# Performance work log

Hardware: AMD Instinct MI355X
Metric: run time of the kernel (lower is better)

The kernel has to match this reference:

```python
import jax, jax.numpy as jnp
import numpy as np

A = 20.0  # sigmoid sharpness used by the module

def norm_sigmoid(x):
    # module's sigmoid: min/max normalize over the whole tensor, then steep sigmoid
    xn = (x - jnp.min(x)) / (jnp.max(x) - jnp.min(x))
    return jax.nn.sigmoid(A * xn)

def setup_inputs() -> dict:
    key = jax.random.key(0)
    ks = jax.random.split(key, 10)
    B, T = 2048, 512
    input_dim, nh1, nh2, nh3, output_dim = 1, 256, 256, 128, 1
    def lin(k, fan_in, fan_out):
        bound = 1.0 / np.sqrt(fan_in)
        kw, kb = jax.random.split(k)
        W = jax.random.uniform(kw, (fan_out, fan_in), jnp.float32, -bound, bound)
        b = jax.random.uniform(kb, (fan_out,), jnp.float32, -bound, bound)
        return W, b
    W1, b1 = lin(ks[0], input_dim, nh1)
    W2, b2 = lin(ks[1], nh1, nh2)
    W4, b4 = lin(ks[2], nh3, output_dim)
    j_w = jax.random.normal(ks[3], (nh3,), jnp.float32)
    k_w = jax.random.normal(ks[4], (nh3,), jnp.float32)
    X = jax.random.normal(ks[5], (B, T), jnp.float32)
    return {"X": X, "W1": W1, "b1": b1, "W2": W2, "b2": b2,
            "W4": W4, "b4": b4, "j_w": j_w, "k_w": k_w}

def reference(X, W1, b1, W2, b2, W4, b4, j_w, k_w):
    B, T = X.shape
    nh3 = j_w.shape[0]
    xs = jnp.swapaxes(X, 0, 1)[:, :, None]  # [T, B, 1] scalar input per step

    def step(state, x_t):
        out1 = norm_sigmoid(x_t @ W1.T + b1)          # [B, nh1]
        out2 = norm_sigmoid(out1 @ W2.T + b2)         # [B, nh2]
        j, k = out2[:, :nh3], out2[:, nh3:]
        inp_j = norm_sigmoid(j * j_w)
        inp_k = norm_sigmoid(k * k_w)
        new_state = (1.0 - state) * inp_j + (1.0 - inp_k) * state  # flip-flop update
        out4 = norm_sigmoid(new_state @ W4.T + b4)    # [B, 1]
        return new_state, out4

    state0 = jnp.zeros((B, nh3), X.dtype)
    _, ys = jax.lax.scan(step, state0, xs)            # ys: [T, B, 1]
    return jnp.squeeze(jnp.swapaxes(ys, 0, 1), axis=2)  # [B, T]
```

## Files before the change

### kernel.cpp

```cpp
#include <hip/hip_runtime.h>

#define TT 512
#define BB 2048
#define HH 256

typedef _Float16 f16x8 __attribute__((ext_vector_type(8)));
typedef _Float16 f16x4 __attribute__((ext_vector_type(4)));
typedef float f32x4 __attribute__((ext_vector_type(4)));

__device__ __forceinline__ float sigf(float z) {
    return __builtin_amdgcn_rcpf(1.0f + __expf(-z));
}
__device__ __forceinline__ unsigned f2o(float f) {
    unsigned u = __float_as_uint(f);
    return (u & 0x80000000u) ? ~u : (u | 0x80000000u);
}
__device__ __forceinline__ float o2f(unsigned o) {
    unsigned u = (o & 0x80000000u) ? (o & 0x7fffffffu) : ~o;
    return __uint_as_float(u);
}

__global__ __launch_bounds__(256) void k0_stats(const float* __restrict__ X,
                                                const float* __restrict__ W1,
                                                const float* __restrict__ b1,
                                                float* __restrict__ mn1f, float* __restrict__ s1f,
                                                unsigned* __restrict__ colGmn,
                                                unsigned* __restrict__ colGmx,
                                                float2* __restrict__ statep) {
    int t = blockIdx.x, tid = threadIdx.x;
    statep[blockIdx.x * 256 + tid] = make_float2(0.f, 0.f);
    colGmn[(size_t)t * 256 + tid] = 0xFFFFFFFFu;
    colGmx[(size_t)t * 256 + tid] = 0u;
    __shared__ float rmn[256], rmx[256];
    float mn = 3.4e38f, mx = -3.4e38f;
    for (int b = tid; b < BB; b += 256) {
        float v = X[(size_t)b * TT + t];
        mn = fminf(mn, v); mx = fmaxf(mx, v);
    }
    rmn[tid] = mn; rmx[tid] = mx; __syncthreads();
    for (int s = 128; s > 0; s >>= 1) {
        if (tid < s) { rmn[tid] = fminf(rmn[tid], rmn[tid + s]); rmx[tid] = fmaxf(rmx[tid], rmx[tid + s]); }
        __syncthreads();
    }
    float xmn = rmn[0], xmx = rmx[0];
    __syncthreads();
    float w = W1[tid], bb = b1[tid];
    float v0 = w * xmn + bb, v1 = w * xmx + bb;
    rmn[tid] = fminf(v0, v1); rmx[tid] = fmaxf(v0, v1); __syncthreads();
    for (int s = 128; s > 0; s >>= 1) {
        if (tid < s) { rmn[tid] = fminf(rmn[tid], rmn[tid + s]); rmx[tid] = fmaxf(rmx[tid], rmx[tid + s]); }
        __syncthreads();
    }
    if (tid == 0) {
        mn1f[t] = rmn[0];
        s1f[t] = 20.0f / (rmx[0] - rmn[0]);
    }
}

__global__ __launch_bounds__(256) void k0b_cvt(const float* __restrict__ W2,
                                               _Float16* __restrict__ W2hi) {
    int i4 = (blockIdx.x * 256 + threadIdx.x) * 4;
    float4 v = *(const float4*)&W2[i4];
    f16x4 h;
    h[0] = (_Float16)v.x; h[1] = (_Float16)v.y; h[2] = (_Float16)v.z; h[3] = (_Float16)v.w;
    *(f16x4*)&W2hi[i4] = h;
}

__global__ __launch_bounds__(256) void k1_gemm(const float* __restrict__ X,
                                               const float* __restrict__ W1,
                                               const float* __restrict__ b1,
                                               const _Float16* __restrict__ W2h,
                                               const float* __restrict__ b2,
                                               const float* __restrict__ mn1f,
                                               const float* __restrict__ s1f,
                                               float* __restrict__ buf,
                                               unsigned* __restrict__ colGmn,
                                               unsigned* __restrict__ colGmx,
                                               int tbase) {
    int tl = blockIdx.z, t = tbase + tl;
    int bBase = blockIdx.x * 64;
    int tid = threadIdx.x;
    __shared__ __align__(16) _Float16 A[2][64 * 256];
    float* C_lds = (float*)A;
    int lane = tid & 63, w = tid >> 6;
    int l15 = lane & 15, hi2 = lane >> 4;

    {
        int sr = tid >> 2, ks0 = (tid & 3) * 64;
        float xr = X[(size_t)(bBase + sr) * TT + t];
        float mn1 = mn1f[t], s1 = s1f[t];
#pragma unroll
        for (int g = 0; g < 8; ++g) {
            int k = ks0 + g * 8;
            float4 wa = *(const float4*)&W1[k];
            float4 wb = *(const float4*)&W1[k + 4];
            float4 ba = *(const float4*)&b1[k];
            float4 bb = *(const float4*)&b1[k + 4];
            float av[8];
            av[0] = sigf((xr * wa.x + ba.x - mn1) * s1);
            av[1] = sigf((xr * wa.y + ba.y - mn1) * s1);
            av[2] = sigf((xr * wa.z + ba.z - mn1) * s1);
            av[3] = sigf((xr * wa.w + ba.w - mn1) * s1);
            av[4] = sigf((xr * wb.x + bb.x - mn1) * s1);
            av[5] = sigf((xr * wb.y + bb.y - mn1) * s1);
            av[6] = sigf((xr * wb.z + bb.z - mn1) * s1);
            av[7] = sigf((xr * wb.w + bb.w - mn1) * s1);
            f16x8 hv, lv;
#pragma unroll
            for (int u = 0; u < 8; ++u) {
                _Float16 ah = (_Float16)av[u];
                hv[u] = ah;
                lv[u] = (_Float16)(av[u] - (float)ah);
            }
            int kgs = (k >> 3) ^ (sr & 7);
            *(f16x8*)&A[0][sr * 256 + kgs * 8] = hv;
            *(f16x8*)&A[1][sr * 256 + kgs * 8] = lv;
        }
    }
    __syncthreads();

    f32x4 acc[4][4];
#pragma unroll
    for (int i = 0; i < 4; ++i)
#pragma unroll
        for (int j = 0; j < 4; ++j) acc[i][j] = (f32x4)0.0f;

    const _Float16* bp[4];
#pragma unroll
    for (int j = 0; j < 4; ++j)
        bp[j] = W2h + (size_t)(w * 64 + j * 16 + l15) * HH + hi2 * 8;

#pragma unroll
    for (int s = 0; s < 8; ++s) {
        f16x8 bh[4];
#pragma unroll
        for (int j = 0; j < 4; ++j) bh[j] = *(const f16x8*)(bp[j] + s * 32);
#pragma unroll
        for (int i = 0; i < 4; ++i) {
            int row = i * 16 + l15;
            int kgs = (s * 4 + hi2) ^ (row & 7);
            f16x8 ah = *(const f16x8*)&A[0][row * 256 + kgs * 8];
            f16x8 al = *(const f16x8*)&A[1][row * 256 + kgs * 8];
#pragma unroll
            for (int j = 0; j < 4; ++j) {
                acc[i][j] = __builtin_amdgcn_mfma_f32_16x16x32_f16(al, bh[j], acc[i][j], 0, 0, 0);
                acc[i][j] = __builtin_amdgcn_mfma_f32_16x16x32_f16(ah, bh[j], acc[i][j], 0, 0, 0);
            }
        }
    }

    float b2r[4];
#pragma unroll
    for (int j = 0; j < 4; ++j) b2r[j] = b2[w * 64 + j * 16 + l15];
#pragma unroll
    for (int j = 0; j < 4; ++j) {
        float vmn = 3.4e38f, vmx = -3.4e38f;
#pragma unroll
        for (int i = 0; i < 4; ++i)
#pragma unroll
            for (int q = 0; q < 4; ++q) {
                float v = acc[i][j][q] + b2r[j];
                acc[i][j][q] = v;
                vmn = fminf(vmn, v); vmx = fmaxf(vmx, v);
            }
        vmn = fminf(vmn, __shfl_xor(vmn, 16)); vmn = fminf(vmn, __shfl_xor(vmn, 32));
        vmx = fmaxf(vmx, __shfl_xor(vmx, 16)); vmx = fmaxf(vmx, __shfl_xor(vmx, 32));
        if (hi2 == 0) {
            int c = w * 64 + j * 16 + l15;
            atomicMin(&colGmn[(size_t)t * 256 + c], f2o(vmn));
            atomicMax(&colGmx[(size_t)t * 256 + c], f2o(vmx));
        }
    }
    __syncthreads();
#pragma unroll
    for (int i = 0; i < 4; ++i)
#pragma unroll
        for (int j = 0; j < 4; ++j)
#pragma unroll
            for (int q = 0; q < 4; ++q)
                C_lds[(i * 16 + hi2 * 4 + q) * 256 + w * 64 + j * 16 + l15] = acc[i][j][q];
    __syncthreads();
#pragma unroll
    for (int it = 0; it < 16; ++it) {
        int idx = it * 256 + tid;
        int row = idx >> 6, g = idx & 63;
        float4 v = *(const float4*)&C_lds[row * 256 + g * 4];
        *(float4*)&buf[((size_t)tl * BB + bBase + row) * HH + g * 4] = v;
    }
}

__global__ __launch_bounds__(256) void k1b(const unsigned* __restrict__ colGmn,
                                           const unsigned* __restrict__ colGmx,
                                           const float* __restrict__ j_w,
                                           const float* __restrict__ k_w,
                                           float* __restrict__ mn2f, float* __restrict__ s2f,
                                           float* __restrict__ mjf, float* __restrict__ sjf,
                                           float* __restrict__ mkf, float* __restrict__ skf,
                                           int tbase) {
    int t = tbase + blockIdx.x, tid = threadIdx.x;
    __shared__ float ra[256], rb[256];
    float cmn = o2f(colGmn[(size_t)t * 256 + tid]);
    float cmx = o2f(colGmx[(size_t)t * 256 + tid]);
    ra[tid] = cmn; rb[tid] = cmx; __syncthreads();
    for (int s = 128; s > 0; s >>= 1) {
        if (tid < s) { ra[tid] = fminf(ra[tid], ra[tid + s]); rb[tid] = fmaxf(rb[tid], rb[tid + s]); }
        __syncthreads();
    }
    float mn2 = ra[0], mx2 = rb[0];
    float s2 = 20.0f / (mx2 - mn2);
    __syncthreads();
    float wv = (tid < 128) ? j_w[tid] : k_w[tid - 128];
    float ea = sigf((cmn - mn2) * s2) * wv;
    float eb = sigf((cmx - mn2) * s2) * wv;
    ra[tid] = fminf(ea, eb); rb[tid] = fmaxf(ea, eb); __syncthreads();
    for (int s = 64; s > 0; s >>= 1) {
        if ((tid & 127) < s) { ra[tid] = fminf(ra[tid], ra[tid + s]); rb[tid] = fmaxf(rb[tid], rb[tid + s]); }
        __syncthreads();
    }
    if (tid == 0) {
        mn2f[t] = mn2; s2f[t] = s2;
        mjf[t] = ra[0]; sjf[t] = 20.0f / (rb[0] - ra[0]);
    }
    if (tid == 128) {
        mkf[t] = ra[128]; skf[t] = 20.0f / (rb[128] - ra[128]);
    }
}

__global__ __launch_bounds__(256) void k3_scan(const float* __restrict__ buf,
                                               const float* __restrict__ W4,
                                               const float* __restrict__ b4,
                                               const float* __restrict__ mn2f, const float* __restrict__ s2f,
                                               const float* __restrict__ mjf, const float* __restrict__ sjf,
                                               const float* __restrict__ mkf, const float* __restrict__ skf,
                                               const float* __restrict__ j_w, const float* __restrict__ k_w,
                                               float2* __restrict__ statep,
                                               float* __restrict__ out4p,
                                               int tbase, int TC) {
    __shared__ float n2L[512], c2L[512], mjL[512], sjL[512], mkL[512], skL[512];
    int tid = threadIdx.x;
    for (int tl = tid; tl < TC; tl += 256) {
        int t = tbase + tl;
        n2L[tl] = mn2f[t]; c2L[tl] = s2f[t];
        mjL[tl] = mjf[t]; sjL[tl] = sjf[t];
        mkL[tl] = mkf[t]; skL[tl] = skf[t];
    }
    __syncthreads();
    int wave = tid >> 6, lane = tid & 63;
    int b = blockIdx.x * 4 + wave;
    float w40 = W4[2 * lane], w41 = W4[2 * lane + 1];
    float jw0 = j_w[2 * lane], jw1 = j_w[2 * lane + 1];
    float kw0 = k_w[2 * lane], kw1 = k_w[2 * lane + 1];
    float bb4 = b4[0];
    float2 stv = statep[b * 64 + lane];
    float s0 = stv.x, s1v = stv.y;
    const float2* basep = (const float2*)buf;
    const int rowstride = BB * 128;
    int off0 = b * 128 + lane;
    float rsave = 0.f;
    float2 jq[8], kq[8];
#pragma unroll
    for (int u = 0; u < 8; ++u) {
        jq[u] = basep[(size_t)u * rowstride + off0];
        kq[u] = basep[(size_t)u * rowstride + off0 + 64];
    }
    for (int t0 = 0; t0 < TC; t0 += 8) {
#pragma unroll
        for (int u = 0; u < 8; ++u) {
            int tl = t0 + u;
            float2 jp = jq[u], kp = kq[u];
            int tn = tl + 8;
            if (tn < TC) {
                jq[u] = basep[(size_t)tn * rowstride + off0];
                kq[u] = basep[(size_t)tn * rowstride + off0 + 64];
            }
            float n2 = n2L[tl], c2 = c2L[tl];
            float pj0 = sigf((jp.x - n2) * c2) * jw0;
            float pj1 = sigf((jp.y - n2) * c2) * jw1;
            float pk0 = sigf((kp.x - n2) * c2) * kw0;
            float pk1 = sigf((kp.y - n2) * c2) * kw1;
            float ij0 = sigf((pj0 - mjL[tl]) * sjL[tl]);
            float ij1 = sigf((pj1 - mjL[tl]) * sjL[tl]);
            float ik0 = sigf((pk0 - mkL[tl]) * skL[tl]);
            float ik1 = sigf((pk1 - mkL[tl]) * skL[tl]);
            s0 = ij0 + s0 * (1.0f - ij0 - ik0);
            s1v = ij1 + s1v * (1.0f - ij1 - ik1);
            float r = s0 * w40 + s1v * w41;
#pragma unroll
            for (int m = 1; m < 64; m <<= 1) r += __shfl_xor(r, m);
            if (lane == (tl & 63)) rsave = r + bb4;
        }
        if (((t0 + 8) & 63) == 0) {
            int base = t0 + 8 - 64;
            out4p[(size_t)b * TT + tbase + base + lane] = rsave;
        }
    }
    if (TC < 64 && lane < TC) out4p[(size_t)b * TT + tbase + lane] = rsave;
    statep[b * 64 + lane] = make_float2(s0, s1v);
}

__global__ __launch_bounds__(256) void k3b(const float* __restrict__ out4p,
                                           float* __restrict__ mn4f, float* __restrict__ s4f) {
    int t = blockIdx.x, tid = threadIdx.x;
    __shared__ float rmn[256], rmx[256];
    float mn = 3.4e38f, mx = -3.4e38f;
    for (int b = tid; b < BB; b += 256) {
        float v = out4p[(size_t)b * TT + t];
        mn = fminf(mn, v); mx = fmaxf(mx, v);
    }
    rmn[tid] = mn; rmx[tid] = mx; __syncthreads();
    for (int s = 128; s > 0; s >>= 1) {
        if (tid < s) { rmn[tid] = fminf(rmn[tid], rmn[tid + s]); rmx[tid] = fmaxf(rmx[tid], rmx[tid + s]); }
        __syncthreads();
    }
    if (tid == 0) { mn4f[t] = rmn[0]; s4f[t] = 20.0f / (rmx[0] - rmn[0]); }
}

__global__ __launch_bounds__(256) void k4_final(float* __restrict__ out,
                                                const float* __restrict__ mn4f,
                                                const float* __restrict__ s4f) {
    int i = blockIdx.x * 256 + threadIdx.x;
    float4 v = ((const float4*)out)[i];
    int t0 = (i * 4) & (TT - 1);
    float4 mn = *(const float4*)&mn4f[t0];
    float4 sc = *(const float4*)&s4f[t0];
    float4 r;
    r.x = sigf((v.x - mn.x) * sc.x);
    r.y = sigf((v.y - mn.y) * sc.y);
    r.z = sigf((v.z - mn.z) * sc.z);
    r.w = sigf((v.w - mn.w) * sc.w);
    ((float4*)out)[i] = r;
}

extern "C" void kernel_launch(void* const* d_in, const int* in_sizes, int n_in,
                              void* d_out, int out_size, void* d_ws, size_t ws_size,
                              hipStream_t stream) {
    const float* X  = (const float*)d_in[0];
    const float* W1 = (const float*)d_in[1];
    const float* b1 = (const float*)d_in[2];
    const float* W2 = (const float*)d_in[3];
    const float* b2 = (const float*)d_in[4];
    const float* W4 = (const float*)d_in[5];
    const float* b4 = (const float*)d_in[6];
    const float* j_w = (const float*)d_in[7];
    const float* k_w = (const float*)d_in[8];
    float* out = (float*)d_out;

    const size_t stateB = (size_t)BB * 64 * sizeof(float2);
    const size_t colGB  = (size_t)TT * 256 * 2 * 4;
    const size_t w2hB   = (size_t)HH * HH * 2;
    const size_t statsB = 65536;
    int TC = 512;
    while (TC > 8 && ((size_t)TC * BB * HH * 4 + stateB + colGB + w2hB + statsB) > ws_size) TC >>= 1;
    int NC = TT / TC;

    char* w = (char*)d_ws;
    float* buf = (float*)w;
    size_t off = (size_t)TC * BB * HH * 4;
    float2* statep = (float2*)(w + off); off += stateB;
    unsigned* colGmn = (unsigned*)(w + off); off += colGB / 2;
    unsigned* colGmx = (unsigned*)(w + off); off += colGB / 2;
    _Float16* W2hi = (_Float16*)(w + off); off += w2hB;
    float* fst = (float*)(w + off);
    float* mn1f = fst;        float* s1f = fst + 512;
    float* mn2f = fst + 1024; float* s2f = fst + 1536;
    float* mjf  = fst + 2048; float* sjf = fst + 2560;
    float* mkf  = fst + 3072; float* skf = fst + 3584;
    float* mn4f = fst + 4096; float* s4f = fst + 4608;
    float* out4p = out;

    k0_stats<<<512, 256, 0, stream>>>(X, W1, b1, mn1f, s1f, colGmn, colGmx, statep);
    k0b_cvt<<<64, 256, 0, stream>>>(W2, W2hi);
    for (int c = 0; c < NC; ++c) {
        int tbase = c * TC;
        k1_gemm<<<dim3(BB / 64, 1, TC), 256, 0, stream>>>(X, W1, b1, W2hi, b2, mn1f, s1f,
                                                          buf, colGmn, colGmx, tbase);
        k1b<<<TC, 256, 0, stream>>>(colGmn, colGmx, j_w, k_w, mn2f, s2f, mjf, sjf, mkf, skf, tbase);
        k3_scan<<<512, 256, 0, stream>>>(buf, W4, b4, mn2f, s2f, mjf, sjf, mkf, skf,
                                         j_w, k_w, statep, out4p, tbase, TC);
    }
    k3b<<<512, 256, 0, stream>>>(out4p, mn4f, s4f);
    k4_final<<<1024, 256, 0, stream>>>(out, mn4f, s4f);
}
```

Measured before the change: 973.9 us.

## Split GEMM K-loop into halves to shrink LDS footprint in k1_gemm

The hi/lo fp16 A staging in k1_gemm is cut from 64KB to half size by processing K in two 128-wide halves, each with its own fill, barrier and MFMA pass. The C write-back now goes through LDS in two 128-column rounds with a padded stride of 132 floats. The aim is to fit within about 33KB of LDS so more blocks can be resident per CU, and the padding should also reduce bank conflicts on the C staging. In exchange the kernel gains extra __syncthreads barriers, and only half the waves do the LDS stores in each epilogue round.

Result: no change. 984.0 us (+1.0%).

```diff
diff --git a/kernel.cpp b/kernel.cpp
--- a/kernel.cpp
+++ b/kernel.cpp
@@ -80,18 +80,35 @@
     int tl = blockIdx.z, t = tbase + tl;
     int bBase = blockIdx.x * 64;
     int tid = threadIdx.x;
-    __shared__ __align__(16) _Float16 A[2][64 * 256];
-    float* C_lds = (float*)A;
+    __shared__ __align__(16) char smem[33792];
+    _Float16* A0 = (_Float16*)smem;
+    _Float16* A1 = A0 + 8192;
+    float* C_lds = (float*)smem;
     int lane = tid & 63, w = tid >> 6;
     int l15 = lane & 15, hi2 = lane >> 4;
 
-    {
-        int sr = tid >> 2, ks0 = (tid & 3) * 64;
-        float xr = X[(size_t)(bBase + sr) * TT + t];
-        float mn1 = mn1f[t], s1 = s1f[t];
-#pragma unroll
-        for (int g = 0; g < 8; ++g) {
-            int k = ks0 + g * 8;
+    int sr = tid >> 2, ks0 = (tid & 3) * 32;
+    float xr = X[(size_t)(bBase + sr) * TT + t];
+    float mn1 = mn1f[t], s1 = s1f[t];
+
+    const _Float16* bp[4];
+#pragma unroll
+    for (int j = 0; j < 4; ++j)
+        bp[j] = W2h + (size_t)(w * 64 + j * 16 + l15) * HH + hi2 * 8;
+
+    f32x4 acc[4][4];
+#pragma unroll
+    for (int i = 0; i < 4; ++i)
+#pragma unroll
+        for (int j = 0; j < 4; ++j) acc[i][j] = (f32x4)0.0f;
+
+#pragma unroll
+    for (int kh = 0; kh < 2; ++kh) {
+        if (kh) __syncthreads();
+#pragma unroll
+        for (int g = 0; g < 4; ++g) {
+            int klocal = ks0 + g * 8;
+            int k = kh * 128 + klocal;
             float4 wa = *(const float4*)&W1[k];
             float4 wb = *(const float4*)&W1[k + 4];
             float4 ba = *(const float4*)&b1[k];
@@ -112,39 +129,27 @@
                 hv[u] = ah;
                 lv[u] = (_Float16)(av[u] - (float)ah);
             }
-            int kgs = (k >> 3) ^ (sr & 7);
-            *(f16x8*)&A[0][sr * 256 + kgs * 8] = hv;
-            *(f16x8*)&A[1][sr * 256 + kgs * 8] = lv;
-        }
-    }
-    __syncthreads();
-
-    f32x4 acc[4][4];
-#pragma unroll
-    for (int i = 0; i < 4; ++i)
-#pragma unroll
-        for (int j = 0; j < 4; ++j) acc[i][j] = (f32x4)0.0f;
-
-    const _Float16* bp[4];
-#pragma unroll
-    for (int j = 0; j < 4; ++j)
-        bp[j] = W2h + (size_t)(w * 64 + j * 16 + l15) * HH + hi2 * 8;
-
-#pragma unroll
-    for (int s = 0; s < 8; ++s) {
-        f16x8 bh[4];
-#pragma unroll
-        for (int j = 0; j < 4; ++j) bh[j] = *(const f16x8*)(bp[j] + s * 32);
-#pragma unroll
-        for (int i = 0; i < 4; ++i) {
-            int row = i * 16 + l15;
-            int kgs = (s * 4 + hi2) ^ (row & 7);
-            f16x8 ah = *(const f16x8*)&A[0][row * 256 + kgs * 8];
-            f16x8 al = *(const f16x8*)&A[1][row * 256 + kgs * 8];
-#pragma unroll
-            for (int j = 0; j < 4; ++j) {
-                acc[i][j] = __builtin_amdgcn_mfma_f32_16x16x32_f16(al, bh[j], acc[i][j], 0, 0, 0);
-                acc[i][j] = __builtin_amdgcn_mfma_f32_16x16x32_f16(ah, bh[j], acc[i][j], 0, 0, 0);
+            int kgs = (klocal >> 3) ^ (sr & 7);
+            *(f16x8*)&A0[sr * 128 + kgs * 8] = hv;
+            *(f16x8*)&A1[sr * 128 + kgs * 8] = lv;
+        }
+        __syncthreads();
+#pragma unroll
+        for (int s = 0; s < 4; ++s) {
+            f16x8 bh[4];
+#pragma unroll
+            for (int j = 0; j < 4; ++j) bh[j] = *(const f16x8*)(bp[j] + kh * 128 + s * 32);
+#pragma unroll
+            for (int i = 0; i < 4; ++i) {
+                int row = i * 16 + l15;
+                int kgs = (s * 4 + hi2) ^ (row & 7);
+                f16x8 ah = *(const f16x8*)&A0[row * 128 + kgs * 8];
+                f16x8 al = *(const f16x8*)&A1[row * 128 + kgs * 8];
+#pragma unroll
+                for (int j = 0; j < 4; ++j) {
+                    acc[i][j] = __builtin_amdgcn_mfma_f32_16x16x32_f16(al, bh[j], acc[i][j], 0, 0, 0);
+                    acc[i][j] = __builtin_amdgcn_mfma_f32_16x16x32_f16(ah, bh[j], acc[i][j], 0, 0, 0);
+                }
             }
         }
     }
@@ -171,21 +176,28 @@
             atomicMax(&colGmx[(size_t)t * 256 + c], f2o(vmx));
         }
     }
-    __syncthreads();
-#pragma unroll
-    for (int i = 0; i < 4; ++i)
-#pragma unroll
-        for (int j = 0; j < 4; ++j)
-#pragma unroll
-            for (int q = 0; q < 4; ++q)
-                C_lds[(i * 16 + hi2 * 4 + q) * 256 + w * 64 + j * 16 + l15] = acc[i][j][q];
-    __syncthreads();
-#pragma unroll
-    for (int it = 0; it < 16; ++it) {
-        int idx = it * 256 + tid;
-        int row = idx >> 6, g = idx & 63;
-        float4 v = *(const float4*)&C_lds[row * 256 + g * 4];
-        *(float4*)&buf[((size_t)tl * BB + bBase + row) * HH + g * 4] = v;
+
+#pragma unroll
+    for (int r = 0; r < 2; ++r) {
+        __syncthreads();
+        if ((w >> 1) == r) {
+            int cl0 = (w & 1) * 64;
+#pragma unroll
+            for (int i = 0; i < 4; ++i)
+#pragma unroll
+                for (int j = 0; j < 4; ++j)
+#pragma unroll
+                    for (int q = 0; q < 4; ++q)
+                        C_lds[(i * 16 + hi2 * 4 + q) * 132 + cl0 + j * 16 + l15] = acc[i][j][q];
+        }
+        __syncthreads();
+#pragma unroll
+        for (int it = 0; it < 8; ++it) {
+            int idx = it * 256 + tid;
+            int row = idx >> 5, c4 = idx & 31;
+            float4 v = *(const float4*)&C_lds[row * 132 + c4 * 4];
+            *(float4*)&buf[((size_t)tl * BB + bBase + row) * HH + r * 128 + c4 * 4] = v;
+        }
     }
 }
 
```

## Halve GEMM row tile and store results directly with nontemporal stores

Applied to the files above, without the earlier changes.

Changes the k1_gemm block tile from 64 to 32 batch rows, which doubles the grid and halves the LDS footprint (32KB instead of 64KB) so more blocks can be resident per CU. It also drops the LDS-staged coalesced write-back of the output tile. Instead it writes each accumulator element straight to global memory with nontemporal stores. The direct stores are scattered 4-byte writes (16 consecutive floats per lane group) rather than float4 rows, and each block now loads the W2 fragments for only half as many rows, which lowers reuse.

New measurement: 1.137 ms. +16.8%, slower.

```diff
diff --git a/kernel.cpp b/kernel.cpp
--- a/kernel.cpp
+++ b/kernel.cpp
@@ -78,19 +78,19 @@
                                                unsigned* __restrict__ colGmx,
                                                int tbase) {
     int tl = blockIdx.z, t = tbase + tl;
-    int bBase = blockIdx.x * 64;
+    int bBase = blockIdx.x * 32;
     int tid = threadIdx.x;
-    __shared__ __align__(16) _Float16 A[2][64 * 256];
-    float* C_lds = (float*)A;
+    __shared__ __align__(16) _Float16 A0[32 * 256];
+    __shared__ __align__(16) _Float16 A1[32 * 256];
     int lane = tid & 63, w = tid >> 6;
     int l15 = lane & 15, hi2 = lane >> 4;
 
     {
-        int sr = tid >> 2, ks0 = (tid & 3) * 64;
+        int sr = tid >> 3, ks0 = (tid & 7) * 32;
         float xr = X[(size_t)(bBase + sr) * TT + t];
         float mn1 = mn1f[t], s1 = s1f[t];
 #pragma unroll
-        for (int g = 0; g < 8; ++g) {
+        for (int g = 0; g < 4; ++g) {
             int k = ks0 + g * 8;
             float4 wa = *(const float4*)&W1[k];
             float4 wb = *(const float4*)&W1[k + 4];
@@ -113,15 +113,15 @@
                 lv[u] = (_Float16)(av[u] - (float)ah);
             }
             int kgs = (k >> 3) ^ (sr & 7);
-            *(f16x8*)&A[0][sr * 256 + kgs * 8] = hv;
-            *(f16x8*)&A[1][sr * 256 + kgs * 8] = lv;
+            *(f16x8*)&A0[sr * 256 + kgs * 8] = hv;
+            *(f16x8*)&A1[sr * 256 + kgs * 8] = lv;
         }
     }
     __syncthreads();
 
-    f32x4 acc[4][4];
-#pragma unroll
-    for (int i = 0; i < 4; ++i)
+    f32x4 acc[2][4];
+#pragma unroll
+    for (int i = 0; i < 2; ++i)
 #pragma unroll
         for (int j = 0; j < 4; ++j) acc[i][j] = (f32x4)0.0f;
 
@@ -136,11 +136,11 @@
 #pragma unroll
         for (int j = 0; j < 4; ++j) bh[j] = *(const f16x8*)(bp[j] + s * 32);
 #pragma unroll
-        for (int i = 0; i < 4; ++i) {
+        for (int i = 0; i < 2; ++i) {
             int row = i * 16 + l15;
             int kgs = (s * 4 + hi2) ^ (row & 7);
-            f16x8 ah = *(const f16x8*)&A[0][row * 256 + kgs * 8];
-            f16x8 al = *(const f16x8*)&A[1][row * 256 + kgs * 8];
+            f16x8 ah = *(const f16x8*)&A0[row * 256 + kgs * 8];
+            f16x8 al = *(const f16x8*)&A1[row * 256 + kgs * 8];
 #pragma unroll
             for (int j = 0; j < 4; ++j) {
                 acc[i][j] = __builtin_amdgcn_mfma_f32_16x16x32_f16(al, bh[j], acc[i][j], 0, 0, 0);
@@ -154,38 +154,24 @@
     for (int j = 0; j < 4; ++j) b2r[j] = b2[w * 64 + j * 16 + l15];
 #pragma unroll
     for (int j = 0; j < 4; ++j) {
+        int col = w * 64 + j * 16 + l15;
         float vmn = 3.4e38f, vmx = -3.4e38f;
 #pragma unroll
-        for (int i = 0; i < 4; ++i)
+        for (int i = 0; i < 2; ++i)
 #pragma unroll
             for (int q = 0; q < 4; ++q) {
-                float v = acc[i][j][q] + b2r[j];
-                acc[i][j][q] = v;
-                vmn = fminf(vmn, v); vmx = fmaxf(vmx, v);
+                float x = acc[i][j][q] + b2r[j];
+                int row = i * 16 + hi2 * 4 + q;
+                __builtin_nontemporal_store(x,
+                    &buf[((size_t)tl * BB + bBase + row) * HH + col]);
+                vmn = fminf(vmn, x); vmx = fmaxf(vmx, x);
             }
         vmn = fminf(vmn, __shfl_xor(vmn, 16)); vmn = fminf(vmn, __shfl_xor(vmn, 32));
         vmx = fmaxf(vmx, __shfl_xor(vmx, 16)); vmx = fmaxf(vmx, __shfl_xor(vmx, 32));
         if (hi2 == 0) {
-            int c = w * 64 + j * 16 + l15;
-            atomicMin(&colGmn[(size_t)t * 256 + c], f2o(vmn));
-            atomicMax(&colGmx[(size_t)t * 256 + c], f2o(vmx));
-        }
-    }
-    __syncthreads();
-#pragma unroll
-    for (int i = 0; i < 4; ++i)
-#pragma unroll
-        for (int j = 0; j < 4; ++j)
-#pragma unroll
-            for (int q = 0; q < 4; ++q)
-                C_lds[(i * 16 + hi2 * 4 + q) * 256 + w * 64 + j * 16 + l15] = acc[i][j][q];
-    __syncthreads();
-#pragma unroll
-    for (int it = 0; it < 16; ++it) {
-        int idx = it * 256 + tid;
-        int row = idx >> 6, g = idx & 63;
-        float4 v = *(const float4*)&C_lds[row * 256 + g * 4];
-        *(float4*)&buf[((size_t)tl * BB + bBase + row) * HH + g * 4] = v;
+            atomicMin(&colGmn[(size_t)t * 256 + col], f2o(vmn));
+            atomicMax(&colGmx[(size_t)t * 256 + col], f2o(vmx));
+        }
     }
 }
 
@@ -372,7 +358,7 @@
     k0b_cvt<<<64, 256, 0, stream>>>(W2, W2hi);
     for (int c = 0; c < NC; ++c) {
         int tbase = c * TC;
-        k1_gemm<<<dim3(BB / 64, 1, TC), 256, 0, stream>>>(X, W1, b1, W2hi, b2, mn1f, s1f,
+        k1_gemm<<<dim3(BB / 32, 1, TC), 256, 0, stream>>>(X, W1, b1, W2hi, b2, mn1f, s1f,
                                                           buf, colGmn, colGmx, tbase);
         k1b<<<TC, 256, 0, stream>>>(colGmn, colGmx, j_w, k_w, mn2f, s2f, mjf, sjf, mkf, skf, tbase);
         k3_scan<<<512, 256, 0, stream>>>(buf, W4, b4, mn2f, s2f, mjf, sjf, mkf, skf,
```
